# Performance work log

Hardware: AMD Instinct MI355X
Metric: run time of the kernel (lower is better)

Reference implementation:

```python
import jax, jax.numpy as jnp
import numpy as np

N_SITES = 128
BOND = 64
PHYS = 2
BATCH = 8192
EPS = 1e-30


def setup_inputs() -> dict:
    key = jax.random.key(0)
    k0, k1, k2, k3 = jax.random.split(key, 4)
    std = 1.0 / np.sqrt(BOND)  # default init_std in _normal_init
    return {
        "configurations": jax.random.randint(k0, (BATCH, N_SITES), 0, PHYS),
        "left_tensor": jax.random.normal(k1, (1, PHYS, BOND), jnp.float32) * std,
        "bulk_tensors": jax.random.normal(k2, (N_SITES - 2, BOND, PHYS, BOND), jnp.float32) * std,
        "right_tensor": jax.random.normal(k3, (BOND, PHYS, 1), jnp.float32) * std,
    }


def _log_amplitude_squared(left, bulk, right, configs):
    # left: (1,P,D), bulk: (N-2,D,P,D), right: (D,P,1), configs: (B,N) int
    env = left[0, configs[:, 0], :]                         # (B, D)
    m = jnp.clip(jnp.max(jnp.abs(env), axis=1), EPS, None)  # (B,)
    env = env / m[:, None]
    log_scale = jnp.log(m)

    def step(carry, xs):
        env, ls = carry
        A, v = xs                                # A: (D,P,D), v: (B,)
        sel = A[:, v, :]                         # (D, B, D) gathered matrices
        env = jnp.einsum('bi,ibj->bj', env, sel)  # (B, D) batched matvec
        m = jnp.clip(jnp.max(jnp.abs(env), axis=1), EPS, None)
        env = env / m[:, None]
        return (env, ls + jnp.log(m)), None

    (env, log_scale), _ = jax.lax.scan(
        step, (env, log_scale), (bulk, configs[:, 1:-1].T))

    sel = right[:, configs[:, -1], 0]            # (D, B)
    psi = jnp.einsum('bd,db->b', env, sel)       # (B,) rescaled amplitude
    m = jnp.clip(jnp.abs(psi), EPS, None)
    psi = psi / m
    log_scale = log_scale + jnp.log(m)

    abs2 = jnp.clip(psi * psi, EPS, None)
    return jnp.log(abs2) + 2.0 * log_scale      # (B,) log|Psi(v)|^2


def reference(configurations, left_tensor, bulk_tensors, right_tensor):
    return _log_amplitude_squared(left_tensor, bulk_tensors, right_tensor, configurations)
```

## Files before the change

kernel.cpp:

```cpp
#include <hip/hip_runtime.h>
#include <math.h>
#include <stdint.h>

typedef __attribute__((ext_vector_type(8))) short bf16x8;
typedef __attribute__((ext_vector_type(4))) float f32x4;
typedef __attribute__((ext_vector_type(4))) int   i32x4;
typedef __attribute__((ext_vector_type(2))) int   i32x2;

#define NSITES 128
#define NBULK  126
#define BOND   64
#define BATCH  8192

#define WSITE     49152
#define WMASK_OFF ((size_t)NBULK * (size_t)WSITE)
#define WS_NEED   (WMASK_OFF + (size_t)BATCH * 16)

#define EBUF0   98304
#define EBUF_SZ 12288
#define RED_OFF 122880
#define SMEM_SZ 123392

#define MFMA_BF16 __builtin_amdgcn_mfma_f32_16x16x32_bf16

__global__ void prep_w(const float* __restrict__ bulk, char* __restrict__ wsd) {
    const int s  = blockIdx.x;
    const int t  = threadIdx.x;
    const int j  = t >> 2;
    const int op = t & 3;
    const float* bs = bulk + (size_t)s * 8192 + j;
    char* dsite = wsd + (size_t)s * WSITE;
    #pragma unroll
    for (int v = 0; v < 2; ++v) {
        #pragma unroll
        for (int oo = 0; oo < 2; ++oo) {
            const int o = op * 2 + oo;
            uint h[3][8];
            #pragma unroll
            for (int e = 0; e < 8; ++e) {
                const float x = bs[(o * 8 + e) * 128 + v * 64];
                const uint  u1 = __float_as_uint(x) & 0xffff0000u;
                const float r1 = x - __uint_as_float(u1);
                const uint  u2 = __float_as_uint(r1) & 0xffff0000u;
                const float r2 = r1 - __uint_as_float(u2);
                const uint  u3 = __float_as_uint(r2) & 0xffff0000u;
                h[0][e] = u1; h[1][e] = u2; h[2][e] = u3;
            }
            char* base = dsite + (size_t)j * 128 + ((o ^ (j & 7)) * 16);
            #pragma unroll
            for (int tm = 0; tm < 3; ++tm) {
                i32x4 q;
                q.x = (int)((h[tm][0] >> 16) | (h[tm][1] & 0xffff0000u));
                q.y = (int)((h[tm][2] >> 16) | (h[tm][3] & 0xffff0000u));
                q.z = (int)((h[tm][4] >> 16) | (h[tm][5] & 0xffff0000u));
                q.w = (int)((h[tm][6] >> 16) | (h[tm][7] & 0xffff0000u));
                *(i32x4*)(base + (v * 3 + tm) * 8192) = q;
            }
        }
    }
}

__global__ void prep_mask(const int* __restrict__ cfg, uint* __restrict__ msk) {
    const int w = threadIdx.x >> 6, l = threadIdx.x & 63;
    const int b = blockIdx.x * 2 + (w >> 1);
    const int half = w & 1;
    int idx = half * 64 + l + 1;
    if (idx > 127) idx = 127;
    const int v = cfg[b * NSITES + idx];
    const unsigned long long bal = __ballot(v != 0);
    if (l == 0) {
        msk[b * 4 + half * 2]     = (uint)(bal & 0xffffffffu);
        msk[b * 4 + half * 2 + 1] = (uint)(bal >> 32);
    }
}


#define PUBLISH(PW) do { \
    uint pa_[3][4]; \
    _Pragma("unroll") \
    for (int r = 0; r < 4; ++r) { \
        const float x_ = eg0[r]; \
        const uint  u1_ = __float_as_uint(x_) & 0xffff0000u; \
        const float r1_ = x_ - __uint_as_float(u1_); \
        const uint  u2_ = __float_as_uint(r1_) & 0xffff0000u; \
        const float r2_ = r1_ - __uint_as_float(u2_); \
        pa_[0][r] = u1_; pa_[1][r] = u2_; \
        pa_[2][r] = __float_as_uint(r2_) & 0xffff0000u; \
    } \
    _Pragma("unroll") \
    for (int tm = 0; tm < 3; ++tm) { \
        i32x2 d_; \
        d_.x = (int)((pa_[tm][0] >> 16) | (pa_[tm][1] & 0xffff0000u)); \
        d_.y = (int)((pa_[tm][2] >> 16) | (pa_[tm][3] & 0xffff0000u)); \
        *(i32x2*)(smem + aW[PW] + tm * 2048) = d_; \
    } \
    _Pragma("unroll") \
    for (int r = 0; r < 4; ++r) { \
        const float x_ = eg1[r]; \
        const uint  u1_ = __float_as_uint(x_) & 0xffff0000u; \
        const float r1_ = x_ - __uint_as_float(u1_); \
        const uint  u2_ = __float_as_uint(r1_) & 0xffff0000u; \
        const float r2_ = r1_ - __uint_as_float(u2_); \
        pa_[0][r] = u1_; pa_[1][r] = u2_; \
        pa_[2][r] = __float_as_uint(r2_) & 0xffff0000u; \
    } \
    _Pragma("unroll") \
    for (int tm = 0; tm < 3; ++tm) { \
        i32x2 d_; \
        d_.x = (int)((pa_[tm][0] >> 16) | (pa_[tm][1] & 0xffff0000u)); \
        d_.y = (int)((pa_[tm][2] >> 16) | (pa_[tm][3] & 0xffff0000u)); \
        *(i32x2*)(smem + aW[PW] + 6144 + tm * 2048) = d_; \
    } \
} while (0)

#define MSTEP(TW, TE) \
    _Pragma("unroll") \
    for (int ks = 0; ks < 2; ++ks) { \
        acc00 = MFMA_BF16(Af[0][TW][ks], Bf[0][TE][ks], acc00, 0, 0, 0); \
        acc01 = MFMA_BF16(Af[1][TW][ks], Bf[0][TE][ks], acc01, 0, 0, 0); \
        acc10 = MFMA_BF16(Af[0][TW][ks], Bf[1][TE][ks], acc10, 0, 0, 0); \
        acc11 = MFMA_BF16(Af[1][TW][ks], Bf[1][TE][ks], acc11, 0, 0, 0); \
    }

#define SITE_BODY(S, II, PAR, DO_SCALE, DO_MAX) do { \
  if (w < 4) { \
    bf16x8 Af[2][3][2], Bf[2][3][2]; \
    _Pragma("unroll") for (int vv = 0; vv < 2; ++vv) \
    _Pragma("unroll") for (int tm = 0; tm < 3; ++tm) \
    _Pragma("unroll") for (int ks = 0; ks < 2; ++ks) \
        Af[vv][tm][ks] = *(const bf16x8*)(smem + aA[PAR][ks] + (vv * 3 + tm) * 8192); \
    _Pragma("unroll") for (int gg = 0; gg < 2; ++gg) \
    _Pragma("unroll") for (int tm = 0; tm < 3; ++tm) \
    _Pragma("unroll") for (int ks = 0; ks < 2; ++ks) \
        Bf[gg][tm][ks] = *(const bf16x8*)(smem + aB[PAR][ks] + (gg * 3 + tm) * 2048); \
    f32x4 acc00 = {0.f,0.f,0.f,0.f}, acc01 = {0.f,0.f,0.f,0.f}; \
    f32x4 acc10 = {0.f,0.f,0.f,0.f}, acc11 = {0.f,0.f,0.f,0.f}; \
    __builtin_amdgcn_s_setprio(1); \
    MSTEP(2,0) MSTEP(1,1) MSTEP(0,2) MSTEP(1,0) MSTEP(0,1) MSTEP(0,0) \
    __builtin_amdgcn_s_setprio(0); \
    const bool v0_ = ((mwa >> (II)) & 1u) != 0u; \
    const bool v1_ = ((mwb >> (II)) & 1u) != 0u; \
    eg0.x = v0_ ? acc01.x : acc00.x;  eg0.y = v0_ ? acc01.y : acc00.y; \
    eg0.z = v0_ ? acc01.z : acc00.z;  eg0.w = v0_ ? acc01.w : acc00.w; \
    eg1.x = v1_ ? acc11.x : acc10.x;  eg1.y = v1_ ? acc11.y : acc10.y; \
    eg1.z = v1_ ? acc11.z : acc10.z;  eg1.w = v1_ ? acc11.w : acc10.w; \
    if (DO_SCALE) { \
      f32x4 m4a = *(const f32x4*)(smem + RED_OFF + lb * 16); \
      f32x4 m4b = *(const f32x4*)(smem + RED_OFF + 256 + lb * 16); \
      const float ma = fmaxf(fmaxf(m4a.x, m4a.y), fmaxf(m4a.z, m4a.w)); \
      const float mb = fmaxf(fmaxf(m4b.x, m4b.y), fmaxf(m4b.z, m4b.w)); \
      const int ea = (__float_as_int(ma) >> 23) & 255; \
      const int eb = (__float_as_int(mb) >> 23) & 255; \
      const float sa = __int_as_float((254 - ea) << 23); \
      const float sb = __int_as_float((254 - eb) << 23); \
      ls0 += (float)(ea - 127) * 0.6931471805599453f; \
      ls1 += (float)(eb - 127) * 0.6931471805599453f; \
      eg0.x *= sa; eg0.y *= sa; eg0.z *= sa; eg0.w *= sa; \
      eg1.x *= sb; eg1.y *= sb; eg1.z *= sb; eg1.w *= sb; \
    } \
    if (DO_MAX) { \
      float ma = fmaxf(fmaxf(fabsf(eg0.x), fabsf(eg0.y)), fmaxf(fabsf(eg0.z), fabsf(eg0.w))); \
      float mb = fmaxf(fmaxf(fabsf(eg1.x), fabsf(eg1.y)), fmaxf(fabsf(eg1.z), fabsf(eg1.w))); \
      ma = fmaxf(ma, __shfl_xor(ma, 16)); ma = fmaxf(ma, __shfl_xor(ma, 32)); \
      mb = fmaxf(mb, __shfl_xor(mb, 16)); mb = fmaxf(mb, __shfl_xor(mb, 32)); \
      if (lg == 0) { \
        *(float*)(smem + RED_OFF + lb * 16 + jt * 4) = ma; \
        *(float*)(smem + RED_OFF + 256 + lb * 16 + jt * 4) = mb; \
      } \
    } \
    PUBLISH((PAR) ^ 1); \
  } else if ((S) + 1 < NBULK) { \
    const char* sp_ = ws + (size_t)((S) + 1) * WSITE + (w - 4) * 12288 + l * 16; \
    char* dp_ = smem + (((PAR) ^ 1) * WSITE) + (w - 4) * 12288; \
    _Pragma("unroll") \
    for (int u = 0; u < 12; ++u) \
      __builtin_amdgcn_global_load_lds( \
          (const __attribute__((address_space(1))) void*)(sp_ + u * 1024), \
          (__attribute__((address_space(3))) void*)(dp_ + u * 1024), 16, 0, 0); \
  } \
  __syncthreads(); \
} while (0)

#define RUN_CHUNK(CB, MWE0, MWE1, CNT, SC0, MXE) { \
  const uint mwa = (MWE0), mwb = (MWE1); \
  _Pragma("unroll 1") \
  for (int i2 = 0; i2 < (CNT); i2 += 2) { \
    SITE_BODY((CB) * 32 + i2,     i2,     0, ((SC0) && i2 == 0),           false); \
    SITE_BODY((CB) * 32 + i2 + 1, i2 + 1, 1, false, ((MXE) && i2 == (CNT) - 2)); \
  } \
}

__global__ __launch_bounds__(512, 2) void mps_main(
    const int*   __restrict__ cfg,
    const float* __restrict__ left,
    const float* __restrict__ right,
    const char*  __restrict__ ws,
    float*       __restrict__ out)
{
    extern __shared__ __align__(16) char smem[];
    const int t  = threadIdx.x;
    const int w  = t >> 6, l = t & 63;
    const int lg = l >> 4, lb = l & 15;
    const int jt = w & 3;
    const int bbase = blockIdx.x * 32;
    const int b0 = bbase + lb, b1 = bbase + 16 + lb;

    int aA[2][2], aB[2][2], aW[2];
    {
        const int key = lb & 7;
        const int s0 = ((0 + lg) ^ key) * 16;
        const int s1 = ((4 + lg) ^ key) * 16;
        const int jrow = jt * 16 + lb;
        aA[0][0] = jrow * 128 + s0;   aA[0][1] = jrow * 128 + s1;
        aA[1][0] = aA[0][0] + WSITE;  aA[1][1] = aA[0][1] + WSITE;
        aB[0][0] = EBUF0 + lb * 128 + s0;  aB[0][1] = EBUF0 + lb * 128 + s1;
        aB[1][0] = aB[0][0] + EBUF_SZ;     aB[1][1] = aB[0][1] + EBUF_SZ;
        aW[0] = EBUF0 + lb * 128 + (((jt * 2 + (lg >> 1)) ^ key) * 16) + (lg & 1) * 8;
        aW[1] = aW[0] + EBUF_SZ;
    }

    float ls0 = 0.f, ls1 = 0.f;
    f32x4 eg0 = {0.f,0.f,0.f,0.f}, eg1 = {0.f,0.f,0.f,0.f};
    uint4 vmg0 = {0,0,0,0}, vmg1 = {0,0,0,0};

    if (w < 4) {
        const uint* mp = (const uint*)(ws + WMASK_OFF);
        vmg0 = *(const uint4*)(mp + (size_t)b0 * 4);
        vmg1 = *(const uint4*)(mp + (size_t)b1 * 4);
        const int c00 = cfg[b0 * NSITES], c01 = cfg[b1 * NSITES];
        const int jout = jt * 16 + lg * 4;
        #pragma unroll
        for (int r = 0; r < 4; ++r) {
            eg0[r] = left[c00 * BOND + jout + r];
            eg1[r] = left[c01 * BOND + jout + r];
        }
        PUBLISH(0);
    } else {
        const char* sp_ = ws + (w - 4) * 12288 + l * 16;
        char* dp_ = smem + (w - 4) * 12288;
        #pragma unroll
        for (int u = 0; u < 12; ++u)
            __builtin_amdgcn_global_load_lds(
                (const __attribute__((address_space(1))) void*)(sp_ + u * 1024),
                (__attribute__((address_space(3))) void*)(dp_ + u * 1024), 16, 0, 0);
    }
    __syncthreads();

    RUN_CHUNK(0, vmg0.x, vmg1.x, 32, false, true)
    RUN_CHUNK(1, vmg0.y, vmg1.y, 32, true,  true)
    RUN_CHUNK(2, vmg0.z, vmg1.z, 32, true,  true)
    RUN_CHUNK(3, vmg0.w, vmg1.w, 30, true,  false)

    if (w < 4) {
        const int vl0 = cfg[b0 * NSITES + 127], vl1 = cfg[b1 * NSITES + 127];
        const int jout = jt * 16 + lg * 4;
        float p0 = eg0.x * right[(jout + 0) * 2 + vl0] + eg0.y * right[(jout + 1) * 2 + vl0]
                 + eg0.z * right[(jout + 2) * 2 + vl0] + eg0.w * right[(jout + 3) * 2 + vl0];
        float p1 = eg1.x * right[(jout + 0) * 2 + vl1] + eg1.y * right[(jout + 1) * 2 + vl1]
                 + eg1.z * right[(jout + 2) * 2 + vl1] + eg1.w * right[(jout + 3) * 2 + vl1];
        p0 += __shfl_xor(p0, 16); p0 += __shfl_xor(p0, 32);
        p1 += __shfl_xor(p1, 16); p1 += __shfl_xor(p1, 32);
        if (lg == 0) {
            *(float*)(smem + RED_OFF + lb * 16 + jt * 4) = p0;
            *(float*)(smem + RED_OFF + 256 + lb * 16 + jt * 4) = p1;
        }
    }
    __syncthreads();
    if (w == 0 && l < 16) {
        f32x4 q0 = *(const f32x4*)(smem + RED_OFF + lb * 16);
        f32x4 q1 = *(const f32x4*)(smem + RED_OFF + 256 + lb * 16);
        const float s0 = (q0.x + q0.y) + (q0.z + q0.w);
        const float s1 = (q1.x + q1.y) + (q1.z + q1.w);
        out[b0] = 2.0f * (ls0 + logf(fmaxf(fabsf(s0), 1e-30f)));
        out[b1] = 2.0f * (ls1 + logf(fmaxf(fabsf(s1), 1e-30f)));
    }
}

#define WPB     16
#define TPB     (WPB * 64)
#define SITE_ELTS (BOND * 2 * BOND)

__global__ __launch_bounds__(TPB, 2) void mps_logamp_fp32(
    const int*   __restrict__ cfg, const float* __restrict__ left,
    const float* __restrict__ bulk, const float* __restrict__ right,
    float* __restrict__ out)
{
    __shared__ float Abuf[2][SITE_ELTS];
    __shared__ float envs[WPB][BOND];
    __shared__ int   cfgs[WPB * NSITES];
    const int t = threadIdx.x;
    const int w = t >> 6, l = t & 63;
    const int bbase = blockIdx.x * WPB;
    const int b = bbase + w;
    cfgs[t] = cfg[bbase * NSITES + t];
    cfgs[t + TPB] = cfg[bbase * NSITES + t + TPB];
    { const float4* src = (const float4*)bulk; float4* dst = (float4*)(&Abuf[0][0]);
      dst[t] = src[t]; dst[t + TPB] = src[t + TPB]; }
    __syncthreads();
    const int c0 = cfgs[w * NSITES];
    float e = left[c0 * BOND + l];
    float m = fabsf(e);
    #pragma unroll
    for (int k = 32; k; k >>= 1) m = fmaxf(m, __shfl_xor(m, k));
    m = fmaxf(m, 1e-30f);
    e = e / m;
    float ls = logf(m);
    envs[w][l] = e;
    for (int s = 0; s < NBULK; ++s) {
        const int cur = s & 1, nxt = cur ^ 1;
        const bool pf = (s + 1 < NBULK);
        float4 p0, p1;
        if (pf) { const float4* src = (const float4*)(bulk + (size_t)(s + 1) * SITE_ELTS);
                  p0 = src[t]; p1 = src[t + TPB]; }
        const int v = cfgs[w * NSITES + (s + 1)];
        const float* Ap = &Abuf[cur][v * BOND + l];
        const float* ev = &envs[w][0];
        float acc = 0.0f;
        #pragma unroll
        for (int i = 0; i < BOND; i += 4) {
            const float4 e4 = *(const float4*)(ev + i);
            acc = fmaf(e4.x, Ap[(i + 0) * 128], acc);
            acc = fmaf(e4.y, Ap[(i + 1) * 128], acc);
            acc = fmaf(e4.z, Ap[(i + 2) * 128], acc);
            acc = fmaf(e4.w, Ap[(i + 3) * 128], acc);
        }
        float mm = fabsf(acc);
        #pragma unroll
        for (int k = 32; k; k >>= 1) mm = fmaxf(mm, __shfl_xor(mm, k));
        mm = fmaxf(mm, 1e-30f);
        acc = acc / mm;
        ls += logf(mm);
        if (pf) { float4* dst = (float4*)(&Abuf[nxt][0]); dst[t] = p0; dst[t + TPB] = p1; }
        envs[w][l] = acc;
        e = acc;
        __syncthreads();
    }
    const int vl = cfgs[w * NSITES + (NSITES - 1)];
    float p = e * right[l * 2 + vl];
    #pragma unroll
    for (int k = 32; k; k >>= 1) p += __shfl_xor(p, k);
    const float am = fmaxf(fabsf(p), 1e-30f);
    if (l == 0) out[b] = 2.0f * (ls + logf(am));
}

extern "C" void kernel_launch(void* const* d_in, const int* in_sizes, int n_in,
                              void* d_out, int out_size, void* d_ws, size_t ws_size,
                              hipStream_t stream) {
    const int*   cfg   = (const int*)d_in[0];
    const float* left  = (const float*)d_in[1];
    const float* bulk  = (const float*)d_in[2];
    const float* right = (const float*)d_in[3];
    float*       out   = (float*)d_out;

    if (ws_size >= WS_NEED) {
        hipFuncSetAttribute((const void*)mps_main,
                            hipFuncAttributeMaxDynamicSharedMemorySize, SMEM_SZ);
        hipLaunchKernelGGL(prep_w, dim3(NBULK), dim3(256), 0, stream,
                           bulk, (char*)d_ws);
        hipLaunchKernelGGL(prep_mask, dim3(BATCH / 2), dim3(256), 0, stream,
                           cfg, (uint*)((char*)d_ws + WMASK_OFF));
        hipLaunchKernelGGL(mps_main, dim3(BATCH / 32), dim3(512), SMEM_SZ, stream,
                           cfg, left, right, (const char*)d_ws, out);
    } else {
        hipLaunchKernelGGL(mps_logamp_fp32, dim3(BATCH / WPB), dim3(TPB), 0, stream,
                           cfg, left, bulk, right, out);
    }
}
```

Baseline: 122.5 us.

## Stream MPS site matrices into registers directly, dropping the loader warps

The bulk-tensor workspace is re-laid out in MFMA fragment order so each compute wave can load its A fragments straight from global memory into a double-buffered register set, prefetching the next site while computing the current one. The four loader waves, the LDS copy of site weights and the large shared-memory allocation go away, so blocks use 256 threads and about 25KB of LDS. The aim is to remove LDS staging traffic and free up occupancy. The cost is more register pressure, and global-load latency that now sits directly on the compute waves' critical path at every site step.

New measurement: 125.6 us. 1.03x slower.

```diff
diff --git a/kernel.cpp b/kernel.cpp
--- a/kernel.cpp
+++ b/kernel.cpp
@@ -16,37 +16,37 @@
 #define WMASK_OFF ((size_t)NBULK * (size_t)WSITE)
 #define WS_NEED   (WMASK_OFF + (size_t)BATCH * 16)
 
-#define EBUF0   98304
 #define EBUF_SZ 12288
-#define RED_OFF 122880
-#define SMEM_SZ 123392
+#define RED_OFF 24576
+#define SMEM_SZ 25088
 
 #define MFMA_BF16 __builtin_amdgcn_mfma_f32_16x16x32_bf16
 
 __global__ void prep_w(const float* __restrict__ bulk, char* __restrict__ wsd) {
     const int s  = blockIdx.x;
     const int t  = threadIdx.x;
-    const int j  = t >> 2;
-    const int op = t & 3;
-    const float* bs = bulk + (size_t)s * 8192 + j;
+    const int jt = (t >> 6) & 3;
+    const int l  = t & 63;
+    const int j  = jt * 16 + (l & 15);
+    const int kb0 = (l >> 4) * 8;
+    const float* bs = bulk + (size_t)s * 8192;
     char* dsite = wsd + (size_t)s * WSITE;
     #pragma unroll
-    for (int v = 0; v < 2; ++v) {
+    for (int ks = 0; ks < 2; ++ks) {
+        const int kb = ks * 32 + kb0;
         #pragma unroll
-        for (int oo = 0; oo < 2; ++oo) {
-            const int o = op * 2 + oo;
+        for (int v = 0; v < 2; ++v) {
             uint h[3][8];
             #pragma unroll
             for (int e = 0; e < 8; ++e) {
-                const float x = bs[(o * 8 + e) * 128 + v * 64];
+                const float x = bs[(size_t)(kb + e) * 128 + v * 64 + j];
                 const uint  u1 = __float_as_uint(x) & 0xffff0000u;
                 const float r1 = x - __uint_as_float(u1);
                 const uint  u2 = __float_as_uint(r1) & 0xffff0000u;
                 const float r2 = r1 - __uint_as_float(u2);
-                const uint  u3 = __float_as_uint(r2) & 0xffff0000u;
-                h[0][e] = u1; h[1][e] = u2; h[2][e] = u3;
+                h[0][e] = u1; h[1][e] = u2;
+                h[2][e] = __float_as_uint(r2) & 0xffff0000u;
             }
-            char* base = dsite + (size_t)j * 128 + ((o ^ (j & 7)) * 16);
             #pragma unroll
             for (int tm = 0; tm < 3; ++tm) {
                 i32x4 q;
@@ -54,7 +54,7 @@
                 q.y = (int)((h[tm][2] >> 16) | (h[tm][3] & 0xffff0000u));
                 q.z = (int)((h[tm][4] >> 16) | (h[tm][5] & 0xffff0000u));
                 q.w = (int)((h[tm][6] >> 16) | (h[tm][7] & 0xffff0000u));
-                *(i32x4*)(base + (v * 3 + tm) * 8192) = q;
+                *(i32x4*)(dsite + ((((v*3+tm)*2+ks)*4 + jt) * 1024) + l * 16) = q;
             }
         }
     }
@@ -75,6 +75,16 @@
 }
 
 
+#define PREFETCH_A(S, DBUF) do { \
+    if ((S) < NBULK) { \
+        const char* gp_ = ws + (size_t)(S) * WSITE; \
+        _Pragma("unroll") for (int vv = 0; vv < 2; ++vv) \
+        _Pragma("unroll") for (int tm = 0; tm < 3; ++tm) \
+        _Pragma("unroll") for (int ks = 0; ks < 2; ++ks) \
+            Areg[DBUF][vv][tm][ks] = *(const bf16x8*)(gp_ + aG[vv][tm][ks]); \
+    } \
+} while (0)
+
 #define PUBLISH(PW) do { \
     uint pa_[3][4]; \
     _Pragma("unroll") \
@@ -113,31 +123,26 @@
     } \
 } while (0)
 
-#define MSTEP(TW, TE) \
+#define MSTEP(TW, TE, PAR) \
     _Pragma("unroll") \
     for (int ks = 0; ks < 2; ++ks) { \
-        acc00 = MFMA_BF16(Af[0][TW][ks], Bf[0][TE][ks], acc00, 0, 0, 0); \
-        acc01 = MFMA_BF16(Af[1][TW][ks], Bf[0][TE][ks], acc01, 0, 0, 0); \
-        acc10 = MFMA_BF16(Af[0][TW][ks], Bf[1][TE][ks], acc10, 0, 0, 0); \
-        acc11 = MFMA_BF16(Af[1][TW][ks], Bf[1][TE][ks], acc11, 0, 0, 0); \
+        acc00 = MFMA_BF16(Areg[PAR][0][TW][ks], Bf[0][TE][ks], acc00, 0, 0, 0); \
+        acc01 = MFMA_BF16(Areg[PAR][1][TW][ks], Bf[0][TE][ks], acc01, 0, 0, 0); \
+        acc10 = MFMA_BF16(Areg[PAR][0][TW][ks], Bf[1][TE][ks], acc10, 0, 0, 0); \
+        acc11 = MFMA_BF16(Areg[PAR][1][TW][ks], Bf[1][TE][ks], acc11, 0, 0, 0); \
     }
 
 #define SITE_BODY(S, II, PAR, DO_SCALE, DO_MAX) do { \
-  if (w < 4) { \
-    bf16x8 Af[2][3][2], Bf[2][3][2]; \
-    _Pragma("unroll") for (int vv = 0; vv < 2; ++vv) \
-    _Pragma("unroll") for (int tm = 0; tm < 3; ++tm) \
-    _Pragma("unroll") for (int ks = 0; ks < 2; ++ks) \
-        Af[vv][tm][ks] = *(const bf16x8*)(smem + aA[PAR][ks] + (vv * 3 + tm) * 8192); \
+    PREFETCH_A((S) + 1, (PAR) ^ 1); \
+    bf16x8 Bf[2][3][2]; \
     _Pragma("unroll") for (int gg = 0; gg < 2; ++gg) \
     _Pragma("unroll") for (int tm = 0; tm < 3; ++tm) \
     _Pragma("unroll") for (int ks = 0; ks < 2; ++ks) \
         Bf[gg][tm][ks] = *(const bf16x8*)(smem + aB[PAR][ks] + (gg * 3 + tm) * 2048); \
     f32x4 acc00 = {0.f,0.f,0.f,0.f}, acc01 = {0.f,0.f,0.f,0.f}; \
     f32x4 acc10 = {0.f,0.f,0.f,0.f}, acc11 = {0.f,0.f,0.f,0.f}; \
-    __builtin_amdgcn_s_setprio(1); \
-    MSTEP(2,0) MSTEP(1,1) MSTEP(0,2) MSTEP(1,0) MSTEP(0,1) MSTEP(0,0) \
-    __builtin_amdgcn_s_setprio(0); \
+    MSTEP(2,0,PAR) MSTEP(1,1,PAR) MSTEP(0,2,PAR) \
+    MSTEP(1,0,PAR) MSTEP(0,1,PAR) MSTEP(0,0,PAR) \
     const bool v0_ = ((mwa >> (II)) & 1u) != 0u; \
     const bool v1_ = ((mwb >> (II)) & 1u) != 0u; \
     eg0.x = v0_ ? acc01.x : acc00.x;  eg0.y = v0_ ? acc01.y : acc00.y; \
@@ -145,52 +150,43 @@
     eg1.x = v1_ ? acc11.x : acc10.x;  eg1.y = v1_ ? acc11.y : acc10.y; \
     eg1.z = v1_ ? acc11.z : acc10.z;  eg1.w = v1_ ? acc11.w : acc10.w; \
     if (DO_SCALE) { \
-      f32x4 m4a = *(const f32x4*)(smem + RED_OFF + lb * 16); \
-      f32x4 m4b = *(const f32x4*)(smem + RED_OFF + 256 + lb * 16); \
-      const float ma = fmaxf(fmaxf(m4a.x, m4a.y), fmaxf(m4a.z, m4a.w)); \
-      const float mb = fmaxf(fmaxf(m4b.x, m4b.y), fmaxf(m4b.z, m4b.w)); \
-      const int ea = (__float_as_int(ma) >> 23) & 255; \
-      const int eb = (__float_as_int(mb) >> 23) & 255; \
-      const float sa = __int_as_float((254 - ea) << 23); \
-      const float sb = __int_as_float((254 - eb) << 23); \
-      ls0 += (float)(ea - 127) * 0.6931471805599453f; \
-      ls1 += (float)(eb - 127) * 0.6931471805599453f; \
-      eg0.x *= sa; eg0.y *= sa; eg0.z *= sa; eg0.w *= sa; \
-      eg1.x *= sb; eg1.y *= sb; eg1.z *= sb; eg1.w *= sb; \
+        f32x4 m4a = *(const f32x4*)(smem + RED_OFF + lb * 16); \
+        f32x4 m4b = *(const f32x4*)(smem + RED_OFF + 256 + lb * 16); \
+        const float ma = fmaxf(fmaxf(m4a.x, m4a.y), fmaxf(m4a.z, m4a.w)); \
+        const float mb = fmaxf(fmaxf(m4b.x, m4b.y), fmaxf(m4b.z, m4b.w)); \
+        const int ea = (__float_as_int(ma) >> 23) & 255; \
+        const int eb = (__float_as_int(mb) >> 23) & 255; \
+        const float sa = __int_as_float((254 - ea) << 23); \
+        const float sb = __int_as_float((254 - eb) << 23); \
+        ls0 += (float)(ea - 127) * 0.6931471805599453f; \
+        ls1 += (float)(eb - 127) * 0.6931471805599453f; \
+        eg0.x *= sa; eg0.y *= sa; eg0.z *= sa; eg0.w *= sa; \
+        eg1.x *= sb; eg1.y *= sb; eg1.z *= sb; eg1.w *= sb; \
     } \
     if (DO_MAX) { \
-      float ma = fmaxf(fmaxf(fabsf(eg0.x), fabsf(eg0.y)), fmaxf(fabsf(eg0.z), fabsf(eg0.w))); \
-      float mb = fmaxf(fmaxf(fabsf(eg1.x), fabsf(eg1.y)), fmaxf(fabsf(eg1.z), fabsf(eg1.w))); \
-      ma = fmaxf(ma, __shfl_xor(ma, 16)); ma = fmaxf(ma, __shfl_xor(ma, 32)); \
-      mb = fmaxf(mb, __shfl_xor(mb, 16)); mb = fmaxf(mb, __shfl_xor(mb, 32)); \
-      if (lg == 0) { \
-        *(float*)(smem + RED_OFF + lb * 16 + jt * 4) = ma; \
-        *(float*)(smem + RED_OFF + 256 + lb * 16 + jt * 4) = mb; \
-      } \
+        float ma = fmaxf(fmaxf(fabsf(eg0.x), fabsf(eg0.y)), fmaxf(fabsf(eg0.z), fabsf(eg0.w))); \
+        float mb = fmaxf(fmaxf(fabsf(eg1.x), fabsf(eg1.y)), fmaxf(fabsf(eg1.z), fabsf(eg1.w))); \
+        ma = fmaxf(ma, __shfl_xor(ma, 16)); ma = fmaxf(ma, __shfl_xor(ma, 32)); \
+        mb = fmaxf(mb, __shfl_xor(mb, 16)); mb = fmaxf(mb, __shfl_xor(mb, 32)); \
+        if (lg == 0) { \
+            *(float*)(smem + RED_OFF + lb * 16 + jt * 4) = ma; \
+            *(float*)(smem + RED_OFF + 256 + lb * 16 + jt * 4) = mb; \
+        } \
     } \
     PUBLISH((PAR) ^ 1); \
-  } else if ((S) + 1 < NBULK) { \
-    const char* sp_ = ws + (size_t)((S) + 1) * WSITE + (w - 4) * 12288 + l * 16; \
-    char* dp_ = smem + (((PAR) ^ 1) * WSITE) + (w - 4) * 12288; \
-    _Pragma("unroll") \
-    for (int u = 0; u < 12; ++u) \
-      __builtin_amdgcn_global_load_lds( \
-          (const __attribute__((address_space(1))) void*)(sp_ + u * 1024), \
-          (__attribute__((address_space(3))) void*)(dp_ + u * 1024), 16, 0, 0); \
-  } \
-  __syncthreads(); \
+    __syncthreads(); \
 } while (0)
 
 #define RUN_CHUNK(CB, MWE0, MWE1, CNT, SC0, MXE) { \
-  const uint mwa = (MWE0), mwb = (MWE1); \
-  _Pragma("unroll 1") \
-  for (int i2 = 0; i2 < (CNT); i2 += 2) { \
-    SITE_BODY((CB) * 32 + i2,     i2,     0, ((SC0) && i2 == 0),           false); \
-    SITE_BODY((CB) * 32 + i2 + 1, i2 + 1, 1, false, ((MXE) && i2 == (CNT) - 2)); \
-  } \
-}
-
-__global__ __launch_bounds__(512, 2) void mps_main(
+    const uint mwa = (MWE0), mwb = (MWE1); \
+    _Pragma("unroll 1") \
+    for (int i2 = 0; i2 < (CNT); i2 += 2) { \
+        SITE_BODY((CB) * 32 + i2,     i2,     0, ((SC0) && i2 == 0),           false); \
+        SITE_BODY((CB) * 32 + i2 + 1, i2 + 1, 1, false, ((MXE) && i2 == (CNT) - 2)); \
+    } \
+}
+
+__global__ __launch_bounds__(256, 1) void mps_main(
     const int*   __restrict__ cfg,
     const float* __restrict__ left,
     const float* __restrict__ right,
@@ -201,49 +197,47 @@
     const int t  = threadIdx.x;
     const int w  = t >> 6, l = t & 63;
     const int lg = l >> 4, lb = l & 15;
-    const int jt = w & 3;
+    const int jt = w;
     const int bbase = blockIdx.x * 32;
     const int b0 = bbase + lb, b1 = bbase + 16 + lb;
 
-    int aA[2][2], aB[2][2], aW[2];
+    int aG[2][3][2];
+    #pragma unroll
+    for (int vv = 0; vv < 2; ++vv)
+        #pragma unroll
+        for (int tm = 0; tm < 3; ++tm)
+            #pragma unroll
+            for (int ks = 0; ks < 2; ++ks)
+                aG[vv][tm][ks] = (((vv*3+tm)*2 + ks)*4 + jt) * 1024 + l * 16;
+
+    int aB[2][2], aW[2];
     {
         const int key = lb & 7;
         const int s0 = ((0 + lg) ^ key) * 16;
         const int s1 = ((4 + lg) ^ key) * 16;
-        const int jrow = jt * 16 + lb;
-        aA[0][0] = jrow * 128 + s0;   aA[0][1] = jrow * 128 + s1;
-        aA[1][0] = aA[0][0] + WSITE;  aA[1][1] = aA[0][1] + WSITE;
-        aB[0][0] = EBUF0 + lb * 128 + s0;  aB[0][1] = EBUF0 + lb * 128 + s1;
+        aB[0][0] = lb * 128 + s0;          aB[0][1] = lb * 128 + s1;
         aB[1][0] = aB[0][0] + EBUF_SZ;     aB[1][1] = aB[0][1] + EBUF_SZ;
-        aW[0] = EBUF0 + lb * 128 + (((jt * 2 + (lg >> 1)) ^ key) * 16) + (lg & 1) * 8;
+        aW[0] = lb * 128 + (((jt * 2 + (lg >> 1)) ^ key) * 16) + (lg & 1) * 8;
         aW[1] = aW[0] + EBUF_SZ;
     }
 
+    bf16x8 Areg[2][2][3][2];
     float ls0 = 0.f, ls1 = 0.f;
     f32x4 eg0 = {0.f,0.f,0.f,0.f}, eg1 = {0.f,0.f,0.f,0.f};
-    uint4 vmg0 = {0,0,0,0}, vmg1 = {0,0,0,0};
-
-    if (w < 4) {
-        const uint* mp = (const uint*)(ws + WMASK_OFF);
-        vmg0 = *(const uint4*)(mp + (size_t)b0 * 4);
-        vmg1 = *(const uint4*)(mp + (size_t)b1 * 4);
-        const int c00 = cfg[b0 * NSITES], c01 = cfg[b1 * NSITES];
-        const int jout = jt * 16 + lg * 4;
-        #pragma unroll
-        for (int r = 0; r < 4; ++r) {
-            eg0[r] = left[c00 * BOND + jout + r];
-            eg1[r] = left[c01 * BOND + jout + r];
-        }
-        PUBLISH(0);
-    } else {
-        const char* sp_ = ws + (w - 4) * 12288 + l * 16;
-        char* dp_ = smem + (w - 4) * 12288;
-        #pragma unroll
-        for (int u = 0; u < 12; ++u)
-            __builtin_amdgcn_global_load_lds(
-                (const __attribute__((address_space(1))) void*)(sp_ + u * 1024),
-                (__attribute__((address_space(3))) void*)(dp_ + u * 1024), 16, 0, 0);
-    }
+
+    PREFETCH_A(0, 0);
+
+    const uint* mp = (const uint*)(ws + WMASK_OFF);
+    uint4 vmg0 = *(const uint4*)(mp + (size_t)b0 * 4);
+    uint4 vmg1 = *(const uint4*)(mp + (size_t)b1 * 4);
+    const int c00 = cfg[b0 * NSITES], c01 = cfg[b1 * NSITES];
+    const int jout = jt * 16 + lg * 4;
+    #pragma unroll
+    for (int r = 0; r < 4; ++r) {
+        eg0[r] = left[c00 * BOND + jout + r];
+        eg1[r] = left[c01 * BOND + jout + r];
+    }
+    PUBLISH(0);
     __syncthreads();
 
     RUN_CHUNK(0, vmg0.x, vmg1.x, 32, false, true)
@@ -251,9 +245,8 @@
     RUN_CHUNK(2, vmg0.z, vmg1.z, 32, true,  true)
     RUN_CHUNK(3, vmg0.w, vmg1.w, 30, true,  false)
 
-    if (w < 4) {
+    {
         const int vl0 = cfg[b0 * NSITES + 127], vl1 = cfg[b1 * NSITES + 127];
-        const int jout = jt * 16 + lg * 4;
         float p0 = eg0.x * right[(jout + 0) * 2 + vl0] + eg0.y * right[(jout + 1) * 2 + vl0]
                  + eg0.z * right[(jout + 2) * 2 + vl0] + eg0.w * right[(jout + 3) * 2 + vl0];
         float p1 = eg1.x * right[(jout + 0) * 2 + vl1] + eg1.y * right[(jout + 1) * 2 + vl1]
@@ -353,13 +346,11 @@
     float*       out   = (float*)d_out;
 
     if (ws_size >= WS_NEED) {
-        hipFuncSetAttribute((const void*)mps_main,
-                            hipFuncAttributeMaxDynamicSharedMemorySize, SMEM_SZ);
         hipLaunchKernelGGL(prep_w, dim3(NBULK), dim3(256), 0, stream,
                            bulk, (char*)d_ws);
         hipLaunchKernelGGL(prep_mask, dim3(BATCH / 2), dim3(256), 0, stream,
                            cfg, (uint*)((char*)d_ws + WMASK_OFF));
-        hipLaunchKernelGGL(mps_main, dim3(BATCH / 32), dim3(512), SMEM_SZ, stream,
+        hipLaunchKernelGGL(mps_main, dim3(BATCH / 32), dim3(256), SMEM_SZ, stream,
                            cfg, left, right, (const char*)d_ws, out);
     } else {
         hipLaunchKernelGGL(mps_logamp_fp32, dim3(BATCH / WPB), dim3(TPB), 0, stream,
```
